# Kernel tuning notes

Hardware: AMD Instinct MI355X
Metric: run time of the kernel (lower is better)

Reference implementation:

```python
import jax, jax.numpy as jnp
import numpy as np

B = 8192
N_IN = 1024
N_OUT = 1024
IN_OUT = N_IN + N_OUT


def setup_inputs() -> dict:
    key = jax.random.key(0)
    ks = jax.random.split(key, 11)
    s = 1.0 / np.sqrt(IN_OUT)  # nn.Linear default init scale
    inp = {
        "x": jax.random.normal(ks[0], (B, N_IN), dtype=jnp.float32),
        "out_tm1": jax.random.normal(ks[1], (B, N_OUT), dtype=jnp.float32),
        "state_tm1": jax.random.normal(ks[2], (B, N_OUT), dtype=jnp.float32),
        "Wf": jax.random.uniform(ks[3], (IN_OUT, N_OUT), jnp.float32, -s, s),
        "bf": jax.random.uniform(ks[4], (N_OUT,), jnp.float32, -s, s),
        "Wi": jax.random.uniform(ks[5], (IN_OUT, N_OUT), jnp.float32, -s, s),
        "bi": jax.random.uniform(ks[6], (N_OUT,), jnp.float32, -s, s),
        "Wc": jax.random.uniform(ks[7], (IN_OUT, N_OUT), jnp.float32, -s, s),
        "bc": jax.random.uniform(ks[8], (N_OUT,), jnp.float32, -s, s),
        "Wo": jax.random.uniform(ks[9], (IN_OUT, N_OUT), jnp.float32, -s, s),
        "bo": jax.random.uniform(ks[10], (N_OUT,), jnp.float32, -s, s),
    }
    return inp


def reference(x, out_tm1, state_tm1, Wf, bf, Wi, bi, Wc, bc, Wo, bo):
    xh = jnp.concatenate((x, out_tm1), axis=-1)  # [B, n_in+n_out]
    f = jax.nn.sigmoid(xh @ Wf + bf)             # forget gate
    i = jax.nn.sigmoid(xh @ Wi + bi)             # input gate
    c = jnp.tanh(xh @ Wc + bc)                   # candidates
    o = jax.nn.sigmoid(xh @ Wo + bo)             # output gate
    new_state = state_tm1 * f + i * c
    output_t = o * jnp.tanh(new_state)
    return (output_t, new_state)
```

## Files before the change

kernel.cpp:

```cpp
#include <hip/hip_runtime.h>

#define B_DIM 8192
#define NOUT  1024
#define KDIM  2048
#define SLOT  24576

typedef __bf16 bf16x8 __attribute__((ext_vector_type(8)));
typedef float  f32x4  __attribute__((ext_vector_type(4)));

__device__ __forceinline__ unsigned short f2bf(float f) {
  unsigned int u = __float_as_uint(f);
  u += 0x7fff + ((u >> 16) & 1);
  return (unsigned short)(u >> 16);
}
__device__ __forceinline__ float sigmoid_f(float x) {
  return 1.0f / (1.0f + __expf(-x));
}
__device__ __forceinline__ float tanh_f(float x) {
  return 1.0f - 2.0f / (__expf(2.0f * x) + 1.0f);
}
__device__ __forceinline__ void gload_lds16(const void* g, void* l) {
  __builtin_amdgcn_global_load_lds(
      (const __attribute__((address_space(1))) void*)g,
      (__attribute__((address_space(3))) void*)l, 16, 0, 0);
}

__device__ __forceinline__ int cimap(int g, int n) {
  return ((n >> 4) << 6) | ((g & 3) << 4) | (n & 15);
}

__global__ void pack_xh_kernel(const float* __restrict__ x,
                               const float* __restrict__ h,
                               unsigned short* __restrict__ xh) {
  const long total = (long)B_DIM * KDIM / 4;
  for (long i = (long)blockIdx.x * blockDim.x + threadIdx.x; i < total;
       i += (long)gridDim.x * blockDim.x) {
    long e = i * 4;
    int b = (int)(e >> 11);
    int c = (int)(e & 2047);
    float4 v = (c < 1024)
        ? *reinterpret_cast<const float4*>(x + (long)b * 1024 + c)
        : *reinterpret_cast<const float4*>(h + (long)b * 1024 + (c - 1024));
    ushort4 o;
    o.x = f2bf(v.x); o.y = f2bf(v.y); o.z = f2bf(v.z); o.w = f2bf(v.w);
    *reinterpret_cast<ushort4*>(xh + e) = o;
  }
}

__global__ void transpose_w_kernel(const float* __restrict__ Wf,
                                   const float* __restrict__ Wi,
                                   const float* __restrict__ Wc,
                                   const float* __restrict__ Wo,
                                   unsigned short* __restrict__ wt) {
  __shared__ float tile[32][33];
  const int g = blockIdx.z;
  const float* W = (g == 0) ? Wf : (g == 1) ? Wi : (g == 2) ? Wc : Wo;
  const int n0 = blockIdx.x * 32;
  const int k0 = blockIdx.y * 32;
  const int tx = threadIdx.x, ty = threadIdx.y;
#pragma unroll
  for (int r = ty; r < 32; r += 8)
    tile[r][tx] = W[(long)(k0 + r) * NOUT + n0 + tx];
  __syncthreads();
#pragma unroll
  for (int r = ty; r < 32; r += 8) {
    int ci = cimap(g, n0 + r);
    wt[(long)ci * KDIM + k0 + tx] = f2bf(tile[tx][r]);
  }
}

#define SB() __builtin_amdgcn_sched_barrier(0);

#define LOAD_FRAGS(S)                                                       \
  _Pragma("unroll") for (int mi = 0; mi < 8; ++mi)                          \
    af[mi] = *reinterpret_cast<const bf16x8*>(                              \
        lds + (S)*SLOT + mi * 1024 + laneRC);                               \
  _Pragma("unroll") for (int ni = 0; ni < 4; ++ni)                          \
    bq[ni] = *reinterpret_cast<const bf16x8*>(                              \
        lds + (S)*SLOT + 8192 + wn * 4096 + ni * 1024 + laneRC);

#define STAGE6(WS, KT) {                                                    \
  const long kb_ = (long)(KT) * 64 + scol;                                  \
  const char* ab_ = xh_b + (m0 + srow0) * 4096 + kb_;                       \
  const char* bb_ = wt_b + (c0 + srow0) * 4096 + kb_;                       \
  gload_lds16(ab_,             lds + (WS)*SLOT +         t16);              \
  gload_lds16(ab_ +  64L*4096, lds + (WS)*SLOT + 4096  + t16);              \
  gload_lds16(bb_,             lds + (WS)*SLOT + 8192  + t16);              \
  gload_lds16(bb_ +  64L*4096, lds + (WS)*SLOT + 12288 + t16);              \
  gload_lds16(bb_ + 128L*4096, lds + (WS)*SLOT + 16384 + t16);              \
  gload_lds16(bb_ + 192L*4096, lds + (WS)*SLOT + 20480 + t16); }

#define MFMA32()                                                            \
  _Pragma("unroll") for (int mi = 0; mi < 8; ++mi)                          \
  _Pragma("unroll") for (int ni = 0; ni < 4; ++ni)                          \
    acc[mi][ni] = __builtin_amdgcn_mfma_f32_16x16x32_bf16(                  \
        af[mi], bq[ni], acc[mi][ni], 0, 0, 0);

#define ITER(RS, WS, KT)                                                    \
  STAGE6(WS, KT)                                                            \
  LOAD_FRAGS(RS)                                                            \
  __builtin_amdgcn_s_setprio(1);                                            \
  MFMA32()                                                                  \
  __builtin_amdgcn_s_setprio(0);                                            \
  asm volatile("s_waitcnt vmcnt(6)" ::: "memory");                          \
  SB()                                                                      \
  __builtin_amdgcn_s_barrier();                                             \
  SB()

__global__ __launch_bounds__(256, 2)
void lstm_gemm_kernel(const unsigned short* __restrict__ xh,
                      const unsigned short* __restrict__ wt,
                      const float* __restrict__ state,
                      const float* __restrict__ bfp,
                      const float* __restrict__ bip,
                      const float* __restrict__ bcp,
                      const float* __restrict__ bop,
                      float* __restrict__ out) {
  __shared__ __attribute__((aligned(128))) char lds[73728];

  const int tid  = threadIdx.x;
  const int lane = tid & 63;
  const int wn   = tid >> 6;

  const int wgid = blockIdx.y * 16 + blockIdx.x;
  const int swz  = (wgid & 7) * 128 + (wgid >> 3);
  const int by   = swz >> 4;
  const int bx   = swz & 15;
  const long m0  = (long)by * 128;
  const long c0  = (long)bx * 256;

  const int key    = (lane >> 1) & 7;
  const int slotsw = (((lane & 1) << 2) | (lane >> 4)) ^ key;
  const int laneRC = key * 128 + slotsw * 16;

  const int vsw   = (tid & 7) ^ ((tid >> 3) & 7);
  const int srow0 = ((tid >> 3) << 1) + (vsw >> 2);
  const int scol  = (vsw & 3) << 4;
  const int t16   = tid * 16;

  const char* xh_b = (const char*)xh;
  const char* wt_b = (const char*)wt;

  f32x4  acc[8][4] = {};
  bf16x8 af[8];
  bf16x8 bq[4];

  STAGE6(0, 0)
  STAGE6(1, 1)
  asm volatile("s_waitcnt vmcnt(6)" ::: "memory");
  SB()
  __builtin_amdgcn_s_barrier();
  SB()

  for (int t = 0; t < 63; t += 3) {
    const int k3 = (t + 3 > 63) ? 63 : t + 3;
    const int k4 = (t + 4 > 63) ? 63 : t + 4;
    ITER(0, 2, t + 2)
    ITER(1, 0, k3)
    ITER(2, 1, k4)
  }
  LOAD_FRAGS(0)
  __builtin_amdgcn_s_setprio(1);
  MFMA32()
  __builtin_amdgcn_s_setprio(0);
  asm volatile("s_waitcnt vmcnt(0) lgkmcnt(0)" ::: "memory");
  SB()

  const int   nout = (bx * 4 + wn) * 16 + (lane & 15);
  const int   rsub4 = (lane >> 4) << 2;
  const float bfv = bfp[nout], biv = bip[nout];
  const float bcv = bcp[nout], bov = bop[nout];
  float* out2 = out + (long)B_DIM * NOUT;
#pragma unroll
  for (int mi = 0; mi < 8; ++mi)
#pragma unroll
    for (int v = 0; v < 4; ++v) {
      const long row = m0 + mi * 16 + rsub4 + v;
      float fg = sigmoid_f(acc[mi][0][v] + bfv);
      float ig = sigmoid_f(acc[mi][1][v] + biv);
      float cg = tanh_f   (acc[mi][2][v] + bcv);
      float og = sigmoid_f(acc[mi][3][v] + bov);
      float st = state[row * NOUT + nout];
      float ns = st * fg + ig * cg;
      out [row * NOUT + nout] = og * tanh_f(ns);
      out2[row * NOUT + nout] = ns;
    }
}

extern "C" void kernel_launch(void* const* d_in, const int* in_sizes, int n_in,
                              void* d_out, int out_size, void* d_ws, size_t ws_size,
                              hipStream_t stream) {
  const float* x     = (const float*)d_in[0];
  const float* h     = (const float*)d_in[1];
  const float* state = (const float*)d_in[2];
  const float* Wf    = (const float*)d_in[3];
  const float* bfp   = (const float*)d_in[4];
  const float* Wi    = (const float*)d_in[5];
  const float* bip   = (const float*)d_in[6];
  const float* Wc    = (const float*)d_in[7];
  const float* bcp   = (const float*)d_in[8];
  const float* Wo    = (const float*)d_in[9];
  const float* bop   = (const float*)d_in[10];
  float* out = (float*)d_out;

  unsigned short* xh = (unsigned short*)d_ws;
  unsigned short* wt = (unsigned short*)((char*)d_ws + (size_t)B_DIM * KDIM * 2);

  hipLaunchKernelGGL(pack_xh_kernel, dim3(2048), dim3(256), 0, stream, x, h, xh);
  hipLaunchKernelGGL(transpose_w_kernel, dim3(NOUT / 32, KDIM / 32, 4),
                     dim3(32, 8), 0, stream, Wf, Wi, Wc, Wo, wt);
  hipLaunchKernelGGL(lstm_gemm_kernel, dim3(16, 64), dim3(256), 0, stream,
                     xh, wt, state, bfp, bip, bcp, bop, out);
}
```

Before: 175.4 us.

## Rewrite LSTM GEMM with 32x32 MFMA, larger tiles and pre-swizzled operand layouts

The pack and weight-transpose kernels now write operands directly in MFMA fragment order, so tiles can be copied to LDS without swizzle arithmetic. The GEMM moves from 256-thread blocks with 128x256 tiles and 16x16x32 MFMA to 512-thread blocks with 256x256 tiles and 32x32x16 MFMA. It double-buffers 64 KB LDS stages, splits each step into two halves, and uses a lane shuffle in the epilogue to pair gate values. The aim is more data reuse and fewer LDS reads per MFMA. In exchange it needs 128 KB of LDS per block and adds shuffle work in the epilogue.

```diff
diff --git a/kernel.cpp b/kernel.cpp
--- a/kernel.cpp
+++ b/kernel.cpp
@@ -3,10 +3,10 @@
 #define B_DIM 8192
 #define NOUT  1024
 #define KDIM  2048
-#define SLOT  24576
 
 typedef __bf16 bf16x8 __attribute__((ext_vector_type(8)));
-typedef float  f32x4  __attribute__((ext_vector_type(4)));
+typedef float  f32x16 __attribute__((ext_vector_type(16)));
+typedef unsigned short u16x8 __attribute__((ext_vector_type(8)));
 
 __device__ __forceinline__ unsigned short f2bf(float f) {
   unsigned int u = __float_as_uint(f);
@@ -25,25 +25,27 @@
       (__attribute__((address_space(3))) void*)l, 16, 0, 0);
 }
 
-__device__ __forceinline__ int cimap(int g, int n) {
-  return ((n >> 4) << 6) | ((g & 3) << 4) | (n & 15);
-}
 
 __global__ void pack_xh_kernel(const float* __restrict__ x,
                                const float* __restrict__ h,
-                               unsigned short* __restrict__ xh) {
-  const long total = (long)B_DIM * KDIM / 4;
-  for (long i = (long)blockIdx.x * blockDim.x + threadIdx.x; i < total;
-       i += (long)gridDim.x * blockDim.x) {
-    long e = i * 4;
-    int b = (int)(e >> 11);
-    int c = (int)(e & 2047);
-    float4 v = (c < 1024)
-        ? *reinterpret_cast<const float4*>(x + (long)b * 1024 + c)
-        : *reinterpret_cast<const float4*>(h + (long)b * 1024 + (c - 1024));
-    ushort4 o;
-    o.x = f2bf(v.x); o.y = f2bf(v.y); o.z = f2bf(v.z); o.w = f2bf(v.w);
-    *reinterpret_cast<ushort4*>(xh + e) = o;
+                               unsigned short* __restrict__ xh_t) {
+  const int total = 1 << 21;
+  for (int u = blockIdx.x * blockDim.x + threadIdx.x; u < total;
+       u += gridDim.x * blockDim.x) {
+    const int l  = u & 63;
+    const int ks = (u >> 6) & 3;
+    const int kt = (u >> 8) & 31;
+    const int Q  = u >> 13;
+    const long row = Q * 32 + (l & 31);
+    const int  k0  = kt * 64 + ks * 16 + (l >> 5) * 8;
+    const float* src = (k0 < 1024) ? (x + row * 1024 + k0)
+                                   : (h + row * 1024 + (k0 - 1024));
+    const float4 v0 = *reinterpret_cast<const float4*>(src);
+    const float4 v1 = *reinterpret_cast<const float4*>(src + 4);
+    u16x8 o;
+    o[0] = f2bf(v0.x); o[1] = f2bf(v0.y); o[2] = f2bf(v0.z); o[3] = f2bf(v0.w);
+    o[4] = f2bf(v1.x); o[5] = f2bf(v1.y); o[6] = f2bf(v1.z); o[7] = f2bf(v1.w);
+    *reinterpret_cast<u16x8*>(xh_t + (long)u * 8) = o;
   }
 }
 
@@ -51,137 +53,166 @@
                                    const float* __restrict__ Wi,
                                    const float* __restrict__ Wc,
                                    const float* __restrict__ Wo,
-                                   unsigned short* __restrict__ wt) {
-  __shared__ float tile[32][33];
-  const int g = blockIdx.z;
+                                   unsigned short* __restrict__ wt_t) {
+  const int P  = blockIdx.x;
+  const int kt = blockIdx.y;
+  const int t  = threadIdx.x;
+  const int ks = t >> 6;
+  const int l  = t & 63;
+  const int col = l & 31;
+  const int g   = ((P & 1) << 1) | (col & 1);
+  const int n   = (P >> 1) * 16 + (col >> 1);
+  const int k0  = kt * 64 + ks * 16 + (l >> 5) * 8;
   const float* W = (g == 0) ? Wf : (g == 1) ? Wi : (g == 2) ? Wc : Wo;
-  const int n0 = blockIdx.x * 32;
-  const int k0 = blockIdx.y * 32;
-  const int tx = threadIdx.x, ty = threadIdx.y;
+  u16x8 o;
 #pragma unroll
-  for (int r = ty; r < 32; r += 8)
-    tile[r][tx] = W[(long)(k0 + r) * NOUT + n0 + tx];
-  __syncthreads();
-#pragma unroll
-  for (int r = ty; r < 32; r += 8) {
-    int ci = cimap(g, n0 + r);
-    wt[(long)ci * KDIM + k0 + tx] = f2bf(tile[tx][r]);
-  }
+  for (int j = 0; j < 8; ++j)
+    o[j] = f2bf(W[(long)(k0 + j) * 1024 + n]);
+  *reinterpret_cast<u16x8*>(
+      wt_t + ((long)(P * 32 + kt) * 4 + ks) * 512 + l * 8) = o;
 }
 
 #define SB() __builtin_amdgcn_sched_barrier(0);
 
-#define LOAD_FRAGS(S)                                                       \
-  _Pragma("unroll") for (int mi = 0; mi < 8; ++mi)                          \
-    af[mi] = *reinterpret_cast<const bf16x8*>(                              \
-        lds + (S)*SLOT + mi * 1024 + laneRC);                               \
-  _Pragma("unroll") for (int ni = 0; ni < 4; ++ni)                          \
-    bq[ni] = *reinterpret_cast<const bf16x8*>(                              \
-        lds + (S)*SLOT + 8192 + wn * 4096 + ni * 1024 + laneRC);
-
-#define STAGE6(WS, KT) {                                                    \
-  const long kb_ = (long)(KT) * 64 + scol;                                  \
-  const char* ab_ = xh_b + (m0 + srow0) * 4096 + kb_;                       \
-  const char* bb_ = wt_b + (c0 + srow0) * 4096 + kb_;                       \
-  gload_lds16(ab_,             lds + (WS)*SLOT +         t16);              \
-  gload_lds16(ab_ +  64L*4096, lds + (WS)*SLOT + 4096  + t16);              \
-  gload_lds16(bb_,             lds + (WS)*SLOT + 8192  + t16);              \
-  gload_lds16(bb_ +  64L*4096, lds + (WS)*SLOT + 12288 + t16);              \
-  gload_lds16(bb_ + 128L*4096, lds + (WS)*SLOT + 16384 + t16);              \
-  gload_lds16(bb_ + 192L*4096, lds + (WS)*SLOT + 20480 + t16); }
-
-#define MFMA32()                                                            \
-  _Pragma("unroll") for (int mi = 0; mi < 8; ++mi)                          \
-  _Pragma("unroll") for (int ni = 0; ni < 4; ++ni)                          \
-    acc[mi][ni] = __builtin_amdgcn_mfma_f32_16x16x32_bf16(                  \
-        af[mi], bq[ni], acc[mi][ni], 0, 0, 0);
-
-#define ITER(RS, WS, KT)                                                    \
-  STAGE6(WS, KT)                                                            \
-  LOAD_FRAGS(RS)                                                            \
-  __builtin_amdgcn_s_setprio(1);                                            \
-  MFMA32()                                                                  \
-  __builtin_amdgcn_s_setprio(0);                                            \
-  asm volatile("s_waitcnt vmcnt(6)" ::: "memory");                          \
-  SB()                                                                      \
-  __builtin_amdgcn_s_barrier();                                             \
-  SB()
-
-__global__ __launch_bounds__(256, 2)
-void lstm_gemm_kernel(const unsigned short* __restrict__ xh,
-                      const unsigned short* __restrict__ wt,
+#define LOAD_AF(BUF, MFB)                                                    \
+  _Pragma("unroll") for (int m2 = 0; m2 < 2; ++m2)                           \
+  _Pragma("unroll") for (int ks = 0; ks < 4; ++ks)                           \
+    af[m2][ks] = *reinterpret_cast<const bf16x8*>(                           \
+        baseA + (BUF)*65536 + ((MFB) + m2) * 4096 + ks * 1024);
+
+#define LOAD_BQ(BUF)                                                         \
+  _Pragma("unroll") for (int nf = 0; nf < 2; ++nf)                           \
+  _Pragma("unroll") for (int ks = 0; ks < 4; ++ks)                           \
+    bq[nf][ks] = *reinterpret_cast<const bf16x8*>(                           \
+        baseB + (BUF)*65536 + nf * 4096 + ks * 1024);
+
+#define MFMA16(MFB)                                                          \
+  _Pragma("unroll") for (int m2 = 0; m2 < 2; ++m2)                           \
+  _Pragma("unroll") for (int nf = 0; nf < 2; ++nf)                           \
+  _Pragma("unroll") for (int ks = 0; ks < 4; ++ks)                           \
+    acc[(MFB) + m2][nf] = __builtin_amdgcn_mfma_f32_32x32x16_bf16(           \
+        af[m2][ks], bq[nf][ks], acc[(MFB) + m2][nf], 0, 0, 0);
+
+#define STAGE_PA(BUF, KT) {                                                  \
+  const char* a_ = srcA_base + (long)(KT) * 4096;                            \
+  gload_lds16(a_,        lds + (BUF)*65536 + dstA0);                         \
+  gload_lds16(a_ + 1024, lds + (BUF)*65536 + dstA0 + 1024);                  \
+  const char* b_ = srcB_base + (long)(KT) * 4096;                            \
+  gload_lds16(b_,        lds + (BUF)*65536 + dstB);                          \
+  gload_lds16(b_ + 1024, lds + (BUF)*65536 + dstB + 1024);                   \
+  gload_lds16(b_ + 2048, lds + (BUF)*65536 + dstB + 2048);                   \
+  gload_lds16(b_ + 3072, lds + (BUF)*65536 + dstB + 3072); }
+
+#define STAGE_PB(BUF, KT) {                                                  \
+  const char* a_ = srcA2_base + (long)(KT) * 4096;                           \
+  gload_lds16(a_,        lds + (BUF)*65536 + dstA2);                         \
+  gload_lds16(a_ + 1024, lds + (BUF)*65536 + dstA2 + 1024); }
+
+#define ITER(BUF, KN)                                                        \
+  LOAD_AF(BUF, 0)                                                            \
+  LOAD_BQ(BUF)                                                               \
+  STAGE_PA(1 - (BUF), KN)                                                    \
+  asm volatile("s_waitcnt vmcnt(6) lgkmcnt(0)" ::: "memory");                \
+  SB() __builtin_amdgcn_s_barrier(); SB()                                    \
+  __builtin_amdgcn_s_setprio(1);                                             \
+  MFMA16(0)                                                                  \
+  __builtin_amdgcn_s_setprio(0);                                             \
+  LOAD_AF(BUF, 2)                                                            \
+  STAGE_PB(1 - (BUF), KN)                                                    \
+  asm volatile("s_waitcnt vmcnt(2) lgkmcnt(0)" ::: "memory");                \
+  SB() __builtin_amdgcn_s_barrier(); SB()                                    \
+  __builtin_amdgcn_s_setprio(1);                                             \
+  MFMA16(2)                                                                  \
+  __builtin_amdgcn_s_setprio(0);
+
+__global__ __launch_bounds__(512, 2)
+void lstm_gemm_kernel(const unsigned short* __restrict__ xh_t,
+                      const unsigned short* __restrict__ wt_t,
                       const float* __restrict__ state,
                       const float* __restrict__ bfp,
                       const float* __restrict__ bip,
                       const float* __restrict__ bcp,
                       const float* __restrict__ bop,
                       float* __restrict__ out) {
-  __shared__ __attribute__((aligned(128))) char lds[73728];
+  __shared__ __attribute__((aligned(128))) char lds[131072];
 
   const int tid  = threadIdx.x;
+  const int w    = tid >> 6;
   const int lane = tid & 63;
-  const int wn   = tid >> 6;
-
-  const int wgid = blockIdx.y * 16 + blockIdx.x;
-  const int swz  = (wgid & 7) * 128 + (wgid >> 3);
-  const int by   = swz >> 4;
-  const int bx   = swz & 15;
-  const long m0  = (long)by * 128;
-  const long c0  = (long)bx * 256;
-
-  const int key    = (lane >> 1) & 7;
-  const int slotsw = (((lane & 1) << 2) | (lane >> 4)) ^ key;
-  const int laneRC = key * 128 + slotsw * 16;
-
-  const int vsw   = (tid & 7) ^ ((tid >> 3) & 7);
-  const int srow0 = ((tid >> 3) << 1) + (vsw >> 2);
-  const int scol  = (vsw & 3) << 4;
-  const int t16   = tid * 16;
-
-  const char* xh_b = (const char*)xh;
-  const char* wt_b = (const char*)wt;
-
-  f32x4  acc[8][4] = {};
-  bf16x8 af[8];
-  bf16x8 bq[4];
-
-  STAGE6(0, 0)
-  STAGE6(1, 1)
-  asm volatile("s_waitcnt vmcnt(6)" ::: "memory");
-  SB()
-  __builtin_amdgcn_s_barrier();
-  SB()
-
-  for (int t = 0; t < 63; t += 3) {
-    const int k3 = (t + 3 > 63) ? 63 : t + 3;
-    const int k4 = (t + 4 > 63) ? 63 : t + 4;
-    ITER(0, 2, t + 2)
-    ITER(1, 0, k3)
-    ITER(2, 1, k4)
+  const int wm   = w >> 2;
+  const int wn   = w & 3;
+  const int l16  = lane * 16;
+
+  int wg = blockIdx.y * 16 + blockIdx.x;
+  wg = (wg & 7) * 64 + (wg >> 3);
+  const int bm = wg >> 4;
+  const int bn = wg & 15;
+  const long m0 = (long)bm * 256;
+
+  const char* baseA = lds + wm * 16384 + l16;
+  const char* baseB = lds + 32768 + wn * 8192 + l16;
+
+  const int sA   = ((w >> 1) < 2) ? (w >> 1) : (w >> 1) + 2;
+  const int ksA0 = (w & 1) * 2;
+  const char* xh_tb = (const char*)xh_t;
+  const char* wt_tb = (const char*)wt_t;
+  const char* srcA_base  = xh_tb + (long)(bm * 8 + sA)     * 131072 + ksA0 * 1024 + l16;
+  const char* srcA2_base = xh_tb + (long)(bm * 8 + sA + 2) * 131072 + ksA0 * 1024 + l16;
+  const char* srcB_base  = wt_tb + (long)(bn * 8 + w)      * 131072 + l16;
+  const int dstA0 = (sA * 4 + ksA0) * 1024;
+  const int dstA2 = ((sA + 2) * 4 + ksA0) * 1024;
+  const int dstB  = 32768 + w * 4096;
+
+  f32x16 acc[4][2] = {};
+  bf16x8 af[2][4];
+  bf16x8 bq[2][4];
+
+  STAGE_PA(0, 0)
+  STAGE_PB(0, 0)
+  asm volatile("s_waitcnt vmcnt(0)" ::: "memory");
+  SB() __builtin_amdgcn_s_barrier(); SB()
+
+  for (int t = 0; t < 32; t += 2) {
+    const int k1 = t + 1;
+    const int k2 = (t + 2 > 31) ? 31 : t + 2;
+    ITER(0, k1)
+    ITER(1, k2)
   }
-  LOAD_FRAGS(0)
-  __builtin_amdgcn_s_setprio(1);
-  MFMA32()
-  __builtin_amdgcn_s_setprio(0);
   asm volatile("s_waitcnt vmcnt(0) lgkmcnt(0)" ::: "memory");
   SB()
 
-  const int   nout = (bx * 4 + wn) * 16 + (lane & 15);
-  const int   rsub4 = (lane >> 4) << 2;
+  const int par = lane & 1;
+  const int kh  = lane >> 5;
+  const int nout = bn * 64 + wn * 16 + ((lane & 31) >> 1);
   const float bfv = bfp[nout], biv = bip[nout];
   const float bcv = bcp[nout], bov = bop[nout];
   float* out2 = out + (long)B_DIM * NOUT;
 #pragma unroll
-  for (int mi = 0; mi < 8; ++mi)
+  for (int mf = 0; mf < 4; ++mf)
 #pragma unroll
-    for (int v = 0; v < 4; ++v) {
-      const long row = m0 + mi * 16 + rsub4 + v;
-      float fg = sigmoid_f(acc[mi][0][v] + bfv);
-      float ig = sigmoid_f(acc[mi][1][v] + biv);
-      float cg = tanh_f   (acc[mi][2][v] + bcv);
-      float og = sigmoid_f(acc[mi][3][v] + bov);
-      float st = state[row * NOUT + nout];
-      float ns = st * fg + ig * cg;
+    for (int rr = 0; rr < 8; ++rr) {
+      const float a0  = acc[mf][0][rr];
+      const float a0h = acc[mf][0][rr + 8];
+      const float a1  = acc[mf][1][rr];
+      const float a1h = acc[mf][1][rr + 8];
+      const float send0 = par ? a0 : a0h;
+      const float keep0 = par ? a0h : a0;
+      const float send1 = par ? a1 : a1h;
+      const float keep1 = par ? a1h : a1;
+      const float oth0 = __shfl_xor(send0, 1, 64);
+      const float oth1 = __shfl_xor(send1, 1, 64);
+      const float fpre = par ? oth0 : keep0;
+      const float ipre = par ? keep0 : oth0;
+      const float cpre = par ? oth1 : keep1;
+      const float opre = par ? keep1 : oth1;
+      const long row = m0 + (wm * 4 + mf) * 32 +
+                       (rr & 3) + 8 * (rr >> 2) + 16 * par + 4 * kh;
+      const float fg = sigmoid_f(fpre + bfv);
+      const float ig = sigmoid_f(ipre + biv);
+      const float cg = tanh_f   (cpre + bcv);
+      const float og = sigmoid_f(opre + bov);
+      const float st = state[row * NOUT + nout];
+      const float ns = st * fg + ig * cg;
       out [row * NOUT + nout] = og * tanh_f(ns);
       out2[row * NOUT + nout] = ns;
     }
@@ -203,12 +234,14 @@
   const float* bop   = (const float*)d_in[10];
   float* out = (float*)d_out;
 
-  unsigned short* xh = (unsigned short*)d_ws;
-  unsigned short* wt = (unsigned short*)((char*)d_ws + (size_t)B_DIM * KDIM * 2);
-
-  hipLaunchKernelGGL(pack_xh_kernel, dim3(2048), dim3(256), 0, stream, x, h, xh);
-  hipLaunchKernelGGL(transpose_w_kernel, dim3(NOUT / 32, KDIM / 32, 4),
-                     dim3(32, 8), 0, stream, Wf, Wi, Wc, Wo, wt);
-  hipLaunchKernelGGL(lstm_gemm_kernel, dim3(16, 64), dim3(256), 0, stream,
-                     xh, wt, state, bfp, bip, bcp, bop, out);
-}
+  unsigned short* xh_t = (unsigned short*)d_ws;
+  unsigned short* wt_t = (unsigned short*)((char*)d_ws +
+                          (size_t)B_DIM * KDIM * 2);
+
+  hipLaunchKernelGGL(pack_xh_kernel, dim3(2048), dim3(256), 0, stream,
+                     x, h, xh_t);
+  hipLaunchKernelGGL(transpose_w_kernel, dim3(128, 32), dim3(256), 0, stream,
+                     Wf, Wi, Wc, Wo, wt_t);
+  hipLaunchKernelGGL(lstm_gemm_kernel, dim3(16, 32), dim3(512), 0, stream,
+                     xh_t, wt_t, state, bfp, bip, bcp, bop, out);
+}
```

New measurement: 171.6 us. -2.2%, faster.
